# Optimization experiments

Measured on AMD Instinct MI355X. Metric: run time of the kernel, lower is better.

The kernel has to match this reference:

```python
import jax, jax.numpy as jnp
import numpy as np
from jax.scipy.special import gammaln

B, T, U = 65536, 64, 8


def gamma_filter(tau, n, T):
    # tau, n: (1, U) already mulFac-scaled. Matches generate_simple_filter_multichan.
    t = jnp.arange(T, dtype=jnp.float32)[:, None]            # (T, 1)
    f = t ** n * jnp.exp(-t / tau)                           # (T, U); f[0]=0 since n>0
    f = f / (tau ** (n + 1.0)) / jnp.exp(gammaln(n + 1.0))
    return f                                                 # (T, U)


def causal_conv(x, K):
    # x: (B, T), K: (T, U). y[b,t,u] = sum_{j<=t} x[b,t-j] * K[j,u]
    # == tf.nn.conv2d with reversed kernel and causal left-pad (T-1, 0).
    T = x.shape[1]
    idx = jnp.arange(T)[:, None] - jnp.arange(T)[None, :]    # (T, T) = t - t'
    Kmat = jnp.where(idx[:, :, None] >= 0, K[jnp.clip(idx, 0, T - 1)], 0.0)  # (T, T, U)
    return jnp.einsum('bs,tsu->btu', x, Kmat)                # (B, T, U)


def setup_inputs() -> dict:
    key = jax.random.key(0)
    ks = jax.random.split(key, 12)
    uni = lambda k, lo, hi: jax.random.uniform(k, (1, U), minval=lo, maxval=hi, dtype=jnp.float32)
    return {
        'inputs': jax.random.uniform(ks[0], (B, T, 1), dtype=jnp.float32),  # light intensity >= 0
        'alpha': uni(ks[1], 0.001, 0.1),
        'beta':  uni(ks[2], 0.001, 0.1),
        'gamma': uni(ks[3], 0.01, 0.1),
        'zeta':  uni(ks[4], 0.0, 0.1),      # computed but unused by call()
        'tauY':  uni(ks[5], 0.001, 0.02),   # y-path is dead code (unused by outputs)
        'nY':    uni(ks[6], 1e-5, 0.1),
        'tauZ':  uni(ks[7], 0.3, 1.0),
        'nZ':    jnp.full((1, U), 0.01, jnp.float32),  # frozen constant in the layer
        'tauC':  uni(ks[8], 0.01, 0.5),
        'nC':    jnp.full((1, U), 0.01, jnp.float32),  # frozen constant in the layer
    }


def reference(inputs, alpha, beta, gamma, zeta, tauY, nY, tauZ, nZ, tauC, nC):
    Bv, Tv, P = inputs.shape  # P == 1 (pixels folded into batch)
    a = alpha * 100.0         # alpha_mulFac
    b = beta * 10.0           # beta_mulFac
    g = gamma * 10.0          # gamma_mulFac
    tau_z = tauZ * 100.0
    n_z = nZ * 10.0
    tau_c = tauC * 100.0
    n_c = nC * 10.0

    Kc = gamma_filter(tau_c, n_c, Tv)                      # (T, U)
    Kz = g[0][None, :] * Kc + (1.0 - g[0][None, :]) * gamma_filter(tau_z, n_z, Tv)

    x = inputs[:, :, 0]                                    # (B, T)
    z = causal_conv(x, Kz)                                 # (B, T, U)

    # slice_tensor: per-unit gather at flat time index (T - argmax_t Kz)
    z_shift = jnp.argmax(Kz, axis=0)                       # (U,), >=1 since Kz[0]=0
    t_idx = jnp.clip(Tv - z_shift, 0, Tv - 1)
    z_sel = z[:, t_idx, jnp.arange(U)]                     # (B, U)

    # outputs = alpha * x / (1 + beta * z), broadcast to (B, T, 1, 1, U)
    out = (a[0][None, None, None, None, :] * inputs[:, :, :, None, None]
           / (1.0 + b[0][None, None, None, None, :] * z_sel[:, None, None, None, :]))
    return out
```

## Files before the change

### kernel.cpp

```cpp
#include <hip/hip_runtime.h>
#include <math.h>

#define TSZ 64
#define USZ 8
#define NB  8
#define XS  68

typedef float nfloat4 __attribute__((ext_vector_type(4)));


__global__ __launch_bounds__(1024) void setup_kernel(const float* __restrict__ alpha,
                             const float* __restrict__ beta,
                             const float* __restrict__ gamma_,
                             const float* __restrict__ tauZ,
                             const float* __restrict__ nZ,
                             const float* __restrict__ tauC,
                             const float* __restrict__ nC,
                             float* __restrict__ ws) {
    __shared__ float kbuf[2][USZ][TSZ];
    __shared__ float kz[USZ][TSZ];
    __shared__ int ti_s[USZ];

    const int tid = threadIdx.x;
    {
        const int fid = tid >> 9;
        const int rem = tid & 511;
        const int u   = rem >> 6;
        const int t   = rem & 63;
        const float tf = (float)t;
        float tau, n;
        if (fid == 0) { tau = tauC[u] * 100.0f; n = nC[u] * 10.0f; }
        else          { tau = tauZ[u] * 100.0f; n = nZ[u] * 10.0f; }
        float f = powf(tf, n) * expf(-tf / tau) / powf(tau, n + 1.0f) / tgammaf(n + 1.0f);
        kbuf[fid][u][t] = f;
    }
    __syncthreads();
    if (tid < 512) {
        const int u = tid >> 6;
        const int t = tid & 63;
        float g = gamma_[u] * 10.0f;
        kz[u][t] = g * kbuf[0][u][t] + (1.0f - g) * kbuf[1][u][t];
    }
    __syncthreads();
    if (tid < USZ) {
        const int u = tid;
        float best = kz[u][0];
        int bi = 0;
        for (int s = 1; s < TSZ; ++s) {
            float v = kz[u][s];
            if (v > best) { best = v; bi = s; }
        }
        int ti = TSZ - bi;
        if (ti > TSZ - 1) ti = TSZ - 1;
        if (ti < 0) ti = 0;
        ti_s[u] = ti;
        ws[512 + u] = alpha[u] * 100.0f;
        ws[520 + u] = beta[u]  * 10.0f;
    }
    __syncthreads();
    if (tid < 512) {
        const int u = tid >> 6;
        const int t = tid & 63;
        int ti = ti_s[u];
        ws[u * TSZ + t] = (t <= ti) ? kz[u][ti - t] : 0.0f;
    }
}

__global__ __launch_bounds__(256) void main_kernel(const float* __restrict__ x,
                                                   const float* __restrict__ ws,
                                                   float* __restrict__ out) {
    __shared__ __attribute__((aligned(16))) float xs[NB * XS];
    __shared__ __attribute__((aligned(16))) float wl[USZ * XS];
    __shared__ __attribute__((aligned(16))) float fs[NB * USZ];

    const int tid = threadIdx.x;
    const int blk = blockIdx.x;

    if (tid < 128) {
        float4 v = ((const float4*)ws)[tid];
        int u  = tid >> 4;
        int s0 = (tid & 15) << 2;
        *((float4*)&wl[u * XS + s0]) = v;
    } else {
        int j = tid - 128;
        const float4* x4 = (const float4*)(x + (size_t)blk * NB * TSZ);
        float4 v = x4[j];
        int bl = j >> 4;
        int s0 = (j & 15) << 2;
        *((float4*)&xs[bl * XS + s0]) = v;
    }
    __syncthreads();

    if (tid < NB * USZ) {
        const int bl = tid >> 3;
        const int u  = tid & 7;
        const float4* xr = (const float4*)&xs[bl * XS];
        const float4* wr = (const float4*)&wl[u * XS];
        float acc = 0.0f;
        #pragma unroll
        for (int j = 0; j < 16; ++j) {
            float4 a = xr[j];
            float4 b = wr[j];
            acc += a.x * b.x + a.y * b.y + a.z * b.z + a.w * b.w;
        }
        float av = ws[512 + u];
        float bv = ws[520 + u];
        fs[bl * USZ + u] = av / (1.0f + bv * acc);
    }
    __syncthreads();

    nfloat4* o4 = (nfloat4*)(out + (size_t)blk * NB * TSZ * USZ);
    #pragma unroll
    for (int k = 0; k < 4; ++k) {
        int j = tid + k * 256;
        int bl   = j >> 7;
        int r    = j & 127;
        int t    = r >> 1;
        int half = r & 1;
        float xv = xs[bl * XS + t];
        float4 f = *((const float4*)&fs[bl * USZ + half * 4]);
        nfloat4 o;
        o.x = xv * f.x; o.y = xv * f.y; o.z = xv * f.z; o.w = xv * f.w;
        __builtin_nontemporal_store(o, &o4[j]);
    }
}

extern "C" void kernel_launch(void* const* d_in, const int* in_sizes, int n_in,
                              void* d_out, int out_size, void* d_ws, size_t ws_size,
                              hipStream_t stream) {
    const float* inputs = (const float*)d_in[0];
    const float* alpha  = (const float*)d_in[1];
    const float* beta   = (const float*)d_in[2];
    const float* gamma_ = (const float*)d_in[3];
    const float* tauZ   = (const float*)d_in[7];
    const float* nZ     = (const float*)d_in[8];
    const float* tauC   = (const float*)d_in[9];
    const float* nC     = (const float*)d_in[10];
    float* out = (float*)d_out;
    float* ws  = (float*)d_ws;

    setup_kernel<<<1, 1024, 0, stream>>>(alpha, beta, gamma_, tauZ, nZ, tauC, nC, ws);

    const int nbatch = in_sizes[0] / TSZ;
    main_kernel<<<nbatch / NB, 256, 0, stream>>>(inputs, ws, out);
}
```

Baseline: 171.3 us.

## Split fused main kernel into separate dot and grid-stride expand kernels

Splits the single fused kernel into two. A dot kernel computes the per-batch scale factors, 32 batches per block with all threads busy, and writes them to workspace. A grid-stride expand kernel then reads x and those factors from global memory and writes the broadcast output. This removes the mostly idle threads in the dot phase and the intra-block serialization, at the cost of an extra launch, a global round trip for the factors, and a second read of x.

```diff
diff --git a/kernel.cpp b/kernel.cpp
--- a/kernel.cpp
+++ b/kernel.cpp
@@ -3,7 +3,7 @@
 
 #define TSZ 64
 #define USZ 8
-#define NB  8
+#define NBA 32
 #define XS  68
 
 typedef float nfloat4 __attribute__((ext_vector_type(4)));
@@ -66,12 +66,10 @@
     }
 }
 
-__global__ __launch_bounds__(256) void main_kernel(const float* __restrict__ x,
-                                                   const float* __restrict__ ws,
-                                                   float* __restrict__ out) {
-    __shared__ __attribute__((aligned(16))) float xs[NB * XS];
+__global__ __launch_bounds__(256) void dot_kernel(const float* __restrict__ x,
+                                                  float* __restrict__ ws) {
+    __shared__ __attribute__((aligned(16))) float xs[NBA * XS];
     __shared__ __attribute__((aligned(16))) float wl[USZ * XS];
-    __shared__ __attribute__((aligned(16))) float fs[NB * USZ];
 
     const int tid = threadIdx.x;
     const int blk = blockIdx.x;
@@ -81,9 +79,11 @@
         int u  = tid >> 4;
         int s0 = (tid & 15) << 2;
         *((float4*)&wl[u * XS + s0]) = v;
-    } else {
-        int j = tid - 128;
-        const float4* x4 = (const float4*)(x + (size_t)blk * NB * TSZ);
+    }
+    const float4* x4 = (const float4*)(x + (size_t)blk * NBA * TSZ);
+    #pragma unroll
+    for (int k = 0; k < 2; ++k) {
+        int j = tid + k * 256;
         float4 v = x4[j];
         int bl = j >> 4;
         int s0 = (j & 15) << 2;
@@ -91,34 +91,35 @@
     }
     __syncthreads();
 
-    if (tid < NB * USZ) {
-        const int bl = tid >> 3;
-        const int u  = tid & 7;
-        const float4* xr = (const float4*)&xs[bl * XS];
-        const float4* wr = (const float4*)&wl[u * XS];
-        float acc = 0.0f;
-        #pragma unroll
-        for (int j = 0; j < 16; ++j) {
-            float4 a = xr[j];
-            float4 b = wr[j];
-            acc += a.x * b.x + a.y * b.y + a.z * b.z + a.w * b.w;
-        }
-        float av = ws[512 + u];
-        float bv = ws[520 + u];
-        fs[bl * USZ + u] = av / (1.0f + bv * acc);
+    const int bl = tid >> 3;
+    const int u  = tid & 7;
+    const float4* xr = (const float4*)&xs[bl * XS];
+    const float4* wr = (const float4*)&wl[u * XS];
+    float acc = 0.0f;
+    #pragma unroll
+    for (int j = 0; j < 16; ++j) {
+        float4 a = xr[j];
+        float4 b = wr[j];
+        acc += a.x * b.x + a.y * b.y + a.z * b.z + a.w * b.w;
     }
-    __syncthreads();
+    float av = ws[512 + u];
+    float bv = ws[520 + u];
+    ws[1024 + blk * (NBA * USZ) + tid] = av / (1.0f + bv * acc);
+}
 
-    nfloat4* o4 = (nfloat4*)(out + (size_t)blk * NB * TSZ * USZ);
-    #pragma unroll
-    for (int k = 0; k < 4; ++k) {
-        int j = tid + k * 256;
-        int bl   = j >> 7;
-        int r    = j & 127;
-        int t    = r >> 1;
-        int half = r & 1;
-        float xv = xs[bl * XS + t];
-        float4 f = *((const float4*)&fs[bl * USZ + half * 4]);
+__global__ __launch_bounds__(256) void expand_kernel(const float* __restrict__ x,
+                                                     const float* __restrict__ fsel,
+                                                     float* __restrict__ out,
+                                                     int total4) {
+    const int stride = gridDim.x * 256;
+    nfloat4* o4 = (nfloat4*)out;
+    for (int j = blockIdx.x * 256 + threadIdx.x; j < total4; j += stride) {
+        int b = j >> 7;
+        int r = j & 127;
+        int t = r >> 1;
+        int h = r & 1;
+        float xv = x[((size_t)b << 6) + t];
+        float4 f = *((const float4*)&fsel[(b << 3) + (h << 2)]);
         nfloat4 o;
         o.x = xv * f.x; o.y = xv * f.y; o.z = xv * f.z; o.w = xv * f.w;
         __builtin_nontemporal_store(o, &o4[j]);
@@ -142,5 +143,8 @@
     setup_kernel<<<1, 1024, 0, stream>>>(alpha, beta, gamma_, tauZ, nZ, tauC, nC, ws);
 
     const int nbatch = in_sizes[0] / TSZ;
-    main_kernel<<<nbatch / NB, 256, 0, stream>>>(inputs, ws, out);
+    dot_kernel<<<nbatch / NBA, 256, 0, stream>>>(inputs, ws);
+
+    const int total4 = nbatch * (TSZ * USZ / 4);
+    expand_kernel<<<4096, 256, 0, stream>>>(inputs, ws + 1024, out, total4);
 }
```

After: 179.3 us. +4.7%, slower.
